# Kernel tuning notes

Measured on AMD Instinct MI355X. Metric: run time of the kernel, lower is better.

## Reference

```python
import jax, jax.numpy as jnp
import numpy as np

TEMPERATURE = 0.07


def setup_inputs() -> dict:
    key = jax.random.key(0)
    k1, k2, k3 = jax.random.split(key, 3)
    b, num_proposals, num_phrases, f = 128, 100, 16, 512
    img_features = jax.random.normal(k1, (b, num_proposals, f), dtype=jnp.float32)
    text_features = jax.random.normal(k2, (b, num_phrases, f), dtype=jnp.float32)
    labels = jax.random.randint(k3, (b, b), 0, 2, dtype=jnp.int64)
    return {"img_features": img_features, "text_features": text_features, "labels": labels}


def reference(img_features, text_features, labels):
    # att_matrix[b,d,t,i] = <text[b,t,:], img[d,i,:]>
    att_matrix = jnp.einsum('btf,dif->bdti', text_features, img_features)
    argmax_box = att_matrix.max(axis=3)        # [b, d, t]  max over proposals
    score_matrix = argmax_box.mean(axis=2)     # [b, d]     mean over phrases
    score_exp = jnp.exp(score_matrix / TEMPERATURE)
    return score_exp
```

## Files before the change

kernel.cpp:

```cpp
#include <hip/hip_runtime.h>
#include <hip/hip_bf16.h>
#include <stdint.h>


typedef __attribute__((ext_vector_type(4))) int   v4i;
typedef __attribute__((ext_vector_type(8))) int   v8i;
typedef __attribute__((ext_vector_type(4))) float f32x4;

constexpr int Bb = 128;
constexpr int P  = 100;
constexpr int T  = 16;
constexpr int F  = 512;
constexpr float TEMP = 0.07f;

constexpr int BM = 128;
constexpr int BK = 128;

__global__ void cvt_kernel(const float4* __restrict__ img, const float4* __restrict__ txt,
                           uint32_t* __restrict__ imgb, uint32_t* __restrict__ txtb,
                           int nimg4, int ntxt4) {
  const int stride = gridDim.x * blockDim.x;
  for (int i = blockIdx.x * blockDim.x + threadIdx.x; i < nimg4; i += stride) {
    float4 v = img[i];
    int w = __builtin_amdgcn_cvt_pk_fp8_f32(v.x, v.y, 0, false);
    w     = __builtin_amdgcn_cvt_pk_fp8_f32(v.z, v.w, w, true);
    imgb[i] = (uint32_t)w;
  }
  for (int i = blockIdx.x * blockDim.x + threadIdx.x; i < ntxt4; i += stride) {
    float4 v = txt[i];
    int w = __builtin_amdgcn_cvt_pk_fp8_f32(v.x, v.y, 0, false);
    w     = __builtin_amdgcn_cvt_pk_fp8_f32(v.z, v.w, w, true);
    txtb[i] = (uint32_t)w;
  }
}

template<bool FUSED>
__global__ __launch_bounds__(256)
void score_kernel(const void* __restrict__ imgp, const void* __restrict__ txtp,
                  float* __restrict__ out) {
  __shared__ __align__(16) unsigned char As[BM * BK];
  __shared__ __align__(16) unsigned char Bs[BM * BK];
  __shared__ float red[BM][2];

  const int d    = blockIdx.x;
  const int b0   = blockIdx.y * (BM / T);
  const int tid  = threadIdx.x;
  const int lane = tid & 63;
  const int w    = tid >> 6;
  const int q    = lane >> 4;
  const int n    = lane & 15;
  const int mh   = w & 1;
  const int nh   = w >> 1;

  f32x4 acc[4][4] = {};

  for (int kk = 0; kk < F; kk += BK) {
    if constexpr (!FUSED) {
      const uint8_t* gi = (const uint8_t*)imgp;
      const uint8_t* gt = (const uint8_t*)txtp;
      const int sub = lane >> 3;
      const int col = (((lane & 7) ^ sub) & 7) * 16;
      #pragma unroll
      for (int rr = 0; rr < 4; rr++) {
        const int c   = rr * 4 + w;
        const int row = c * 8 + sub;
        const uint8_t* ga = gt + (size_t)(b0 * T + row) * F + kk + col;
        __builtin_amdgcn_global_load_lds(
            (const __attribute__((address_space(1))) void*)ga,
            (__attribute__((address_space(3))) void*)&As[c * 1024], 16, 0, 0);
        const int prow = row < P ? row : 0;
        const uint8_t* gb = gi + ((size_t)d * P + prow) * F + kk + col;
        __builtin_amdgcn_global_load_lds(
            (const __attribute__((address_space(1))) void*)gb,
            (__attribute__((address_space(3))) void*)&Bs[c * 1024], 16, 0, 0);
      }
    } else {
      const float* gi = (const float*)imgp;
      const float* gt = (const float*)txtp;
      #pragma unroll
      for (int s = 0; s < 8; s++) {
        const int slot = s * 256 + tid;
        const int row  = slot >> 4;
        const int half = slot & 15;
        const int colf = half * 8;
        const int swz  = ((half >> 1) ^ (row & 7));
        const int offb = row * BK + swz * 16 + (half & 1) * 8;
        float4 v0 = *(const float4*)(gt + (size_t)(b0 * T + row) * F + kk + colf);
        float4 v1 = *(const float4*)(gt + (size_t)(b0 * T + row) * F + kk + colf + 4);
        int w0 = __builtin_amdgcn_cvt_pk_fp8_f32(v0.x, v0.y, 0, false);
        w0     = __builtin_amdgcn_cvt_pk_fp8_f32(v0.z, v0.w, w0, true);
        int w1 = __builtin_amdgcn_cvt_pk_fp8_f32(v1.x, v1.y, 0, false);
        w1     = __builtin_amdgcn_cvt_pk_fp8_f32(v1.z, v1.w, w1, true);
        *(uint2*)&As[offb] = make_uint2((uint32_t)w0, (uint32_t)w1);
        const int prow = row < P ? row : 0;
        float4 u0 = *(const float4*)(gi + ((size_t)d * P + prow) * F + kk + colf);
        float4 u1 = *(const float4*)(gi + ((size_t)d * P + prow) * F + kk + colf + 4);
        int x0 = __builtin_amdgcn_cvt_pk_fp8_f32(u0.x, u0.y, 0, false);
        x0     = __builtin_amdgcn_cvt_pk_fp8_f32(u0.z, u0.w, x0, true);
        int x1 = __builtin_amdgcn_cvt_pk_fp8_f32(u1.x, u1.y, 0, false);
        x1     = __builtin_amdgcn_cvt_pk_fp8_f32(u1.z, u1.w, x1, true);
        *(uint2*)&Bs[offb] = make_uint2((uint32_t)x0, (uint32_t)x1);
      }
    }
    __syncthreads();

    {
      const int k7 = n & 7;
      const int s0 = (2 * q) ^ k7;
      v8i a[4], bfr[4];
      #pragma unroll
      for (int rt = 0; rt < 4; rt++) {
        const int off = (mh * 64 + rt * 16 + n) * BK;
        v4i lo = *(const v4i*)&As[off + s0 * 16];
        v4i hi = *(const v4i*)&As[off + (s0 ^ 1) * 16];
        a[rt] = __builtin_shufflevector(lo, hi, 0, 1, 2, 3, 4, 5, 6, 7);
      }
      #pragma unroll
      for (int ct = 0; ct < 4; ct++) {
        const int off = (nh * 64 + ct * 16 + n) * BK;
        v4i lo = *(const v4i*)&Bs[off + s0 * 16];
        v4i hi = *(const v4i*)&Bs[off + (s0 ^ 1) * 16];
        bfr[ct] = __builtin_shufflevector(lo, hi, 0, 1, 2, 3, 4, 5, 6, 7);
      }
      #pragma unroll
      for (int rt = 0; rt < 4; rt++)
        #pragma unroll
        for (int ct = 0; ct < 4; ct++)
          acc[rt][ct] = __builtin_amdgcn_mfma_scale_f32_16x16x128_f8f6f4(
              a[rt], bfr[ct], acc[rt][ct], 0, 0, 0, 127, 0, 127);
    }
    __syncthreads();
  }

  #pragma unroll
  for (int rt = 0; rt < 4; rt++) {
    float m[4];
    #pragma unroll
    for (int r = 0; r < 4; r++) {
      float v = -3.0e38f;
      #pragma unroll
      for (int ct = 0; ct < 4; ct++) {
        const bool valid = (nh * 64 + ct * 16 + n) < P;
        const float x = acc[rt][ct][r];
        v = valid ? fmaxf(v, x) : v;
      }
      #pragma unroll
      for (int off = 1; off < 16; off <<= 1)
        v = fmaxf(v, __shfl_xor(v, off));
      m[r] = v;
    }
    if (n == 0) {
      #pragma unroll
      for (int r = 0; r < 4; r++)
        red[mh * 64 + rt * 16 + q * 4 + r][nh] = m[r];
    }
  }
  __syncthreads();

  if (tid < BM / T) {
    float s = 0.f;
    #pragma unroll
    for (int t = 0; t < T; t++) {
      const int r = tid * T + t;
      s += fmaxf(red[r][0], red[r][1]);
    }
    const float arg = fminf(s * (1.0f / (T * TEMP)), 88.0f);
    out[(size_t)(b0 + tid) * Bb + d] = expf(arg);
  }
}

extern "C" void kernel_launch(void* const* d_in, const int* in_sizes, int n_in,
                              void* d_out, int out_size, void* d_ws, size_t ws_size,
                              hipStream_t stream) {
  const float* img = (const float*)d_in[0];
  const float* txt = (const float*)d_in[1];
  float* out = (float*)d_out;

  const size_t imgN = (size_t)Bb * P * F;
  const size_t txtN = (size_t)Bb * T * F;
  const size_t need = imgN + txtN;

  dim3 grid(Bb, (Bb * T) / BM);
  if (ws_size >= need) {
    uint8_t* imgb = (uint8_t*)d_ws;
    uint8_t* txtb = imgb + imgN;
    cvt_kernel<<<2048, 256, 0, stream>>>((const float4*)img, (const float4*)txt,
                                         (uint32_t*)imgb, (uint32_t*)txtb,
                                         (int)(imgN / 4), (int)(txtN / 4));
    score_kernel<false><<<grid, 256, 0, stream>>>(imgb, txtb, out);
  } else {
    score_kernel<true><<<grid, 256, 0, stream>>>(img, txt, out);
  }
}
```

Measured before the change: 103.7 us.

## Double-buffer LDS tiles to overlap next K-slice loads with MFMA

```diff
diff --git a/kernel.cpp b/kernel.cpp
--- a/kernel.cpp
+++ b/kernel.cpp
@@ -15,6 +15,7 @@
 
 constexpr int BM = 128;
 constexpr int BK = 128;
+constexpr int NK = F / BK;
 
 __global__ void cvt_kernel(const float4* __restrict__ img, const float4* __restrict__ txt,
                            uint32_t* __restrict__ imgb, uint32_t* __restrict__ txtb,
@@ -38,8 +39,8 @@
 __global__ __launch_bounds__(256)
 void score_kernel(const void* __restrict__ imgp, const void* __restrict__ txtp,
                   float* __restrict__ out) {
-  __shared__ __align__(16) unsigned char As[BM * BK];
-  __shared__ __align__(16) unsigned char Bs[BM * BK];
+  __shared__ __align__(16) unsigned char As[2][BM * BK];
+  __shared__ __align__(16) unsigned char Bs[2][BM * BK];
   __shared__ float red[BM][2];
 
   const int d    = blockIdx.x;
@@ -54,7 +55,7 @@
 
   f32x4 acc[4][4] = {};
 
-  for (int kk = 0; kk < F; kk += BK) {
+  auto stage = [&](int buf, int kk) {
     if constexpr (!FUSED) {
       const uint8_t* gi = (const uint8_t*)imgp;
       const uint8_t* gt = (const uint8_t*)txtp;
@@ -67,12 +68,12 @@
         const uint8_t* ga = gt + (size_t)(b0 * T + row) * F + kk + col;
         __builtin_amdgcn_global_load_lds(
             (const __attribute__((address_space(1))) void*)ga,
-            (__attribute__((address_space(3))) void*)&As[c * 1024], 16, 0, 0);
+            (__attribute__((address_space(3))) void*)&As[buf][c * 1024], 16, 0, 0);
         const int prow = row < P ? row : 0;
         const uint8_t* gb = gi + ((size_t)d * P + prow) * F + kk + col;
         __builtin_amdgcn_global_load_lds(
             (const __attribute__((address_space(1))) void*)gb,
-            (__attribute__((address_space(3))) void*)&Bs[c * 1024], 16, 0, 0);
+            (__attribute__((address_space(3))) void*)&Bs[buf][c * 1024], 16, 0, 0);
       }
     } else {
       const float* gi = (const float*)imgp;
@@ -91,7 +92,7 @@
         w0     = __builtin_amdgcn_cvt_pk_fp8_f32(v0.z, v0.w, w0, true);
         int w1 = __builtin_amdgcn_cvt_pk_fp8_f32(v1.x, v1.y, 0, false);
         w1     = __builtin_amdgcn_cvt_pk_fp8_f32(v1.z, v1.w, w1, true);
-        *(uint2*)&As[offb] = make_uint2((uint32_t)w0, (uint32_t)w1);
+        *(uint2*)&As[buf][offb] = make_uint2((uint32_t)w0, (uint32_t)w1);
         const int prow = row < P ? row : 0;
         float4 u0 = *(const float4*)(gi + ((size_t)d * P + prow) * F + kk + colf);
         float4 u1 = *(const float4*)(gi + ((size_t)d * P + prow) * F + kk + colf + 4);
@@ -99,37 +100,43 @@
         x0     = __builtin_amdgcn_cvt_pk_fp8_f32(u0.z, u0.w, x0, true);
         int x1 = __builtin_amdgcn_cvt_pk_fp8_f32(u1.x, u1.y, 0, false);
         x1     = __builtin_amdgcn_cvt_pk_fp8_f32(u1.z, u1.w, x1, true);
-        *(uint2*)&Bs[offb] = make_uint2((uint32_t)x0, (uint32_t)x1);
+        *(uint2*)&Bs[buf][offb] = make_uint2((uint32_t)x0, (uint32_t)x1);
       }
     }
+  };
+
+  stage(0, 0);
+
+  #pragma unroll
+  for (int k4 = 0; k4 < NK; k4++) {
     __syncthreads();
-
-    {
-      const int k7 = n & 7;
-      const int s0 = (2 * q) ^ k7;
-      v8i a[4], bfr[4];
-      #pragma unroll
-      for (int rt = 0; rt < 4; rt++) {
-        const int off = (mh * 64 + rt * 16 + n) * BK;
-        v4i lo = *(const v4i*)&As[off + s0 * 16];
-        v4i hi = *(const v4i*)&As[off + (s0 ^ 1) * 16];
-        a[rt] = __builtin_shufflevector(lo, hi, 0, 1, 2, 3, 4, 5, 6, 7);
-      }
-      #pragma unroll
-      for (int ct = 0; ct < 4; ct++) {
-        const int off = (nh * 64 + ct * 16 + n) * BK;
-        v4i lo = *(const v4i*)&Bs[off + s0 * 16];
-        v4i hi = *(const v4i*)&Bs[off + (s0 ^ 1) * 16];
-        bfr[ct] = __builtin_shufflevector(lo, hi, 0, 1, 2, 3, 4, 5, 6, 7);
-      }
-      #pragma unroll
-      for (int rt = 0; rt < 4; rt++)
-        #pragma unroll
-        for (int ct = 0; ct < 4; ct++)
-          acc[rt][ct] = __builtin_amdgcn_mfma_scale_f32_16x16x128_f8f6f4(
-              a[rt], bfr[ct], acc[rt][ct], 0, 0, 0, 127, 0, 127);
-    }
-    __syncthreads();
+    if (k4 + 1 < NK) stage((k4 + 1) & 1, (k4 + 1) * BK);
+
+    const unsigned char* Ab = As[k4 & 1];
+    const unsigned char* Bbuf = Bs[k4 & 1];
+    const int k7 = n & 7;
+    const int s0 = (2 * q) ^ k7;
+    v8i a[4], bfr[4];
+    #pragma unroll
+    for (int rt = 0; rt < 4; rt++) {
+      const int off = (mh * 64 + rt * 16 + n) * BK;
+      v4i lo = *(const v4i*)&Ab[off + s0 * 16];
+      v4i hi = *(const v4i*)&Ab[off + (s0 ^ 1) * 16];
+      a[rt] = __builtin_shufflevector(lo, hi, 0, 1, 2, 3, 4, 5, 6, 7);
+    }
+    #pragma unroll
+    for (int ct = 0; ct < 4; ct++) {
+      const int off = (nh * 64 + ct * 16 + n) * BK;
+      v4i lo = *(const v4i*)&Bbuf[off + s0 * 16];
+      v4i hi = *(const v4i*)&Bbuf[off + (s0 ^ 1) * 16];
+      bfr[ct] = __builtin_shufflevector(lo, hi, 0, 1, 2, 3, 4, 5, 6, 7);
+    }
+    #pragma unroll
+    for (int rt = 0; rt < 4; rt++)
+      #pragma unroll
+      for (int ct = 0; ct < 4; ct++)
+        acc[rt][ct] = __builtin_amdgcn_mfma_scale_f32_16x16x128_f8f6f4(
+            a[rt], bfr[ct], acc[rt][ct], 0, 0, 0, 127, 0, 127);
   }
 
   #pragma unroll
```

Measured after the change: 100.5 us. 1.03x faster.

## Load fp8 MFMA operands directly from global memory, bypassing LDS staging

Applied to the files above, without the earlier changes.

```diff
diff --git a/kernel.cpp b/kernel.cpp
--- a/kernel.cpp
+++ b/kernel.cpp
@@ -12,9 +12,6 @@
 constexpr int T  = 16;
 constexpr int F  = 512;
 constexpr float TEMP = 0.07f;
-
-constexpr int BM = 128;
-constexpr int BK = 128;
 
 __global__ void cvt_kernel(const float4* __restrict__ img, const float4* __restrict__ txt,
                            uint32_t* __restrict__ imgb, uint32_t* __restrict__ txtb,
@@ -34,16 +31,12 @@
   }
 }
 
-template<bool FUSED>
 __global__ __launch_bounds__(256)
-void score_kernel(const void* __restrict__ imgp, const void* __restrict__ txtp,
+void score_direct(const uint8_t* __restrict__ gi, const uint8_t* __restrict__ gt,
                   float* __restrict__ out) {
-  __shared__ __align__(16) unsigned char As[BM * BK];
-  __shared__ __align__(16) unsigned char Bs[BM * BK];
-  __shared__ float red[BM][2];
+  __shared__ float red[128][2];
 
   const int d    = blockIdx.x;
-  const int b0   = blockIdx.y * (BM / T);
   const int tid  = threadIdx.x;
   const int lane = tid & 63;
   const int w    = tid >> 6;
@@ -52,84 +45,41 @@
   const int mh   = w & 1;
   const int nh   = w >> 1;
 
+  const uint8_t* aB[4];
+  const uint8_t* bB[4];
+  #pragma unroll
+  for (int rt = 0; rt < 4; rt++)
+    aB[rt] = gt + (size_t)(blockIdx.y * 128 + mh * 64 + rt * 16 + n) * F + q * 32;
+  #pragma unroll
+  for (int ct = 0; ct < 4; ct++) {
+    const int rl   = nh * 64 + ct * 16 + n;
+    const int prow = rl < P ? rl : 0;
+    bB[ct] = gi + ((size_t)d * P + prow) * F + q * 32;
+  }
+
   f32x4 acc[4][4] = {};
 
-  for (int kk = 0; kk < F; kk += BK) {
-    if constexpr (!FUSED) {
-      const uint8_t* gi = (const uint8_t*)imgp;
-      const uint8_t* gt = (const uint8_t*)txtp;
-      const int sub = lane >> 3;
-      const int col = (((lane & 7) ^ sub) & 7) * 16;
-      #pragma unroll
-      for (int rr = 0; rr < 4; rr++) {
-        const int c   = rr * 4 + w;
-        const int row = c * 8 + sub;
-        const uint8_t* ga = gt + (size_t)(b0 * T + row) * F + kk + col;
-        __builtin_amdgcn_global_load_lds(
-            (const __attribute__((address_space(1))) void*)ga,
-            (__attribute__((address_space(3))) void*)&As[c * 1024], 16, 0, 0);
-        const int prow = row < P ? row : 0;
-        const uint8_t* gb = gi + ((size_t)d * P + prow) * F + kk + col;
-        __builtin_amdgcn_global_load_lds(
-            (const __attribute__((address_space(1))) void*)gb,
-            (__attribute__((address_space(3))) void*)&Bs[c * 1024], 16, 0, 0);
-      }
-    } else {
-      const float* gi = (const float*)imgp;
-      const float* gt = (const float*)txtp;
-      #pragma unroll
-      for (int s = 0; s < 8; s++) {
-        const int slot = s * 256 + tid;
-        const int row  = slot >> 4;
-        const int half = slot & 15;
-        const int colf = half * 8;
-        const int swz  = ((half >> 1) ^ (row & 7));
-        const int offb = row * BK + swz * 16 + (half & 1) * 8;
-        float4 v0 = *(const float4*)(gt + (size_t)(b0 * T + row) * F + kk + colf);
-        float4 v1 = *(const float4*)(gt + (size_t)(b0 * T + row) * F + kk + colf + 4);
-        int w0 = __builtin_amdgcn_cvt_pk_fp8_f32(v0.x, v0.y, 0, false);
-        w0     = __builtin_amdgcn_cvt_pk_fp8_f32(v0.z, v0.w, w0, true);
-        int w1 = __builtin_amdgcn_cvt_pk_fp8_f32(v1.x, v1.y, 0, false);
-        w1     = __builtin_amdgcn_cvt_pk_fp8_f32(v1.z, v1.w, w1, true);
-        *(uint2*)&As[offb] = make_uint2((uint32_t)w0, (uint32_t)w1);
-        const int prow = row < P ? row : 0;
-        float4 u0 = *(const float4*)(gi + ((size_t)d * P + prow) * F + kk + colf);
-        float4 u1 = *(const float4*)(gi + ((size_t)d * P + prow) * F + kk + colf + 4);
-        int x0 = __builtin_amdgcn_cvt_pk_fp8_f32(u0.x, u0.y, 0, false);
-        x0     = __builtin_amdgcn_cvt_pk_fp8_f32(u0.z, u0.w, x0, true);
-        int x1 = __builtin_amdgcn_cvt_pk_fp8_f32(u1.x, u1.y, 0, false);
-        x1     = __builtin_amdgcn_cvt_pk_fp8_f32(u1.z, u1.w, x1, true);
-        *(uint2*)&Bs[offb] = make_uint2((uint32_t)x0, (uint32_t)x1);
-      }
-    }
-    __syncthreads();
-
-    {
-      const int k7 = n & 7;
-      const int s0 = (2 * q) ^ k7;
-      v8i a[4], bfr[4];
-      #pragma unroll
-      for (int rt = 0; rt < 4; rt++) {
-        const int off = (mh * 64 + rt * 16 + n) * BK;
-        v4i lo = *(const v4i*)&As[off + s0 * 16];
-        v4i hi = *(const v4i*)&As[off + (s0 ^ 1) * 16];
-        a[rt] = __builtin_shufflevector(lo, hi, 0, 1, 2, 3, 4, 5, 6, 7);
-      }
-      #pragma unroll
-      for (int ct = 0; ct < 4; ct++) {
-        const int off = (nh * 64 + ct * 16 + n) * BK;
-        v4i lo = *(const v4i*)&Bs[off + s0 * 16];
-        v4i hi = *(const v4i*)&Bs[off + (s0 ^ 1) * 16];
-        bfr[ct] = __builtin_shufflevector(lo, hi, 0, 1, 2, 3, 4, 5, 6, 7);
-      }
-      #pragma unroll
-      for (int rt = 0; rt < 4; rt++)
-        #pragma unroll
-        for (int ct = 0; ct < 4; ct++)
-          acc[rt][ct] = __builtin_amdgcn_mfma_scale_f32_16x16x128_f8f6f4(
-              a[rt], bfr[ct], acc[rt][ct], 0, 0, 0, 127, 0, 127);
-    }
-    __syncthreads();
+  #pragma unroll
+  for (int kk = 0; kk < F; kk += 128) {
+    v8i a[4], b[4];
+    #pragma unroll
+    for (int rt = 0; rt < 4; rt++) {
+      v4i lo = *(const v4i*)(aB[rt] + kk);
+      v4i hi = *(const v4i*)(aB[rt] + kk + 16);
+      a[rt] = __builtin_shufflevector(lo, hi, 0, 1, 2, 3, 4, 5, 6, 7);
+    }
+    #pragma unroll
+    for (int ct = 0; ct < 4; ct++) {
+      v4i lo = *(const v4i*)(bB[ct] + kk);
+      v4i hi = *(const v4i*)(bB[ct] + kk + 16);
+      b[ct] = __builtin_shufflevector(lo, hi, 0, 1, 2, 3, 4, 5, 6, 7);
+    }
+    #pragma unroll
+    for (int rt = 0; rt < 4; rt++)
+      #pragma unroll
+      for (int ct = 0; ct < 4; ct++)
+        acc[rt][ct] = __builtin_amdgcn_mfma_scale_f32_16x16x128_f8f6f4(
+            a[rt], b[ct], acc[rt][ct], 0, 0, 0, 127, 0, 127);
   }
 
   #pragma unroll
@@ -157,7 +107,116 @@
   }
   __syncthreads();
 
-  if (tid < BM / T) {
+  if (tid < 8) {
+    float s = 0.f;
+    #pragma unroll
+    for (int t = 0; t < T; t++) {
+      const int r = tid * T + t;
+      s += fmaxf(red[r][0], red[r][1]);
+    }
+    const float arg = fminf(s * (1.0f / (T * TEMP)), 88.0f);
+    out[(size_t)(blockIdx.y * 8 + tid) * Bb + d] = expf(arg);
+  }
+}
+
+__global__ __launch_bounds__(256)
+void score_fallback(const float* __restrict__ gi, const float* __restrict__ gt,
+                    float* __restrict__ out) {
+  __shared__ __align__(16) unsigned char As[128 * 128];
+  __shared__ __align__(16) unsigned char Bs[128 * 128];
+  __shared__ float red[128][2];
+
+  const int d    = blockIdx.x;
+  const int b0   = blockIdx.y * 8;
+  const int tid  = threadIdx.x;
+  const int lane = tid & 63;
+  const int q    = lane >> 4;
+  const int n    = lane & 15;
+  const int w    = tid >> 6;
+  const int mh   = w & 1;
+  const int nh   = w >> 1;
+
+  f32x4 acc[4][4] = {};
+
+  for (int kk = 0; kk < F; kk += 128) {
+    #pragma unroll
+    for (int s = 0; s < 8; s++) {
+      const int slot = s * 256 + tid;
+      const int row  = slot >> 4;
+      const int half = slot & 15;
+      const int colf = half * 8;
+      const int swz  = ((half >> 1) ^ (row & 7));
+      const int offb = row * 128 + swz * 16 + (half & 1) * 8;
+      float4 v0 = *(const float4*)(gt + (size_t)(b0 * T + row) * F + kk + colf);
+      float4 v1 = *(const float4*)(gt + (size_t)(b0 * T + row) * F + kk + colf + 4);
+      int w0 = __builtin_amdgcn_cvt_pk_fp8_f32(v0.x, v0.y, 0, false);
+      w0     = __builtin_amdgcn_cvt_pk_fp8_f32(v0.z, v0.w, w0, true);
+      int w1 = __builtin_amdgcn_cvt_pk_fp8_f32(v1.x, v1.y, 0, false);
+      w1     = __builtin_amdgcn_cvt_pk_fp8_f32(v1.z, v1.w, w1, true);
+      *(uint2*)&As[offb] = make_uint2((uint32_t)w0, (uint32_t)w1);
+      const int prow = row < P ? row : 0;
+      float4 u0 = *(const float4*)(gi + ((size_t)d * P + prow) * F + kk + colf);
+      float4 u1 = *(const float4*)(gi + ((size_t)d * P + prow) * F + kk + colf + 4);
+      int x0 = __builtin_amdgcn_cvt_pk_fp8_f32(u0.x, u0.y, 0, false);
+      x0     = __builtin_amdgcn_cvt_pk_fp8_f32(u0.z, u0.w, x0, true);
+      int x1 = __builtin_amdgcn_cvt_pk_fp8_f32(u1.x, u1.y, 0, false);
+      x1     = __builtin_amdgcn_cvt_pk_fp8_f32(u1.z, u1.w, x1, true);
+      *(uint2*)&Bs[offb] = make_uint2((uint32_t)x0, (uint32_t)x1);
+    }
+    __syncthreads();
+
+    const int k7 = n & 7;
+    const int s0 = (2 * q) ^ k7;
+    v8i a[4], bfr[4];
+    #pragma unroll
+    for (int rt = 0; rt < 4; rt++) {
+      const int off = (mh * 64 + rt * 16 + n) * 128;
+      v4i lo = *(const v4i*)&As[off + s0 * 16];
+      v4i hi = *(const v4i*)&As[off + (s0 ^ 1) * 16];
+      a[rt] = __builtin_shufflevector(lo, hi, 0, 1, 2, 3, 4, 5, 6, 7);
+    }
+    #pragma unroll
+    for (int ct = 0; ct < 4; ct++) {
+      const int off = (nh * 64 + ct * 16 + n) * 128;
+      v4i lo = *(const v4i*)&Bs[off + s0 * 16];
+      v4i hi = *(const v4i*)&Bs[off + (s0 ^ 1) * 16];
+      bfr[ct] = __builtin_shufflevector(lo, hi, 0, 1, 2, 3, 4, 5, 6, 7);
+    }
+    #pragma unroll
+    for (int rt = 0; rt < 4; rt++)
+      #pragma unroll
+      for (int ct = 0; ct < 4; ct++)
+        acc[rt][ct] = __builtin_amdgcn_mfma_scale_f32_16x16x128_f8f6f4(
+            a[rt], bfr[ct], acc[rt][ct], 0, 0, 0, 127, 0, 127);
+    __syncthreads();
+  }
+
+  #pragma unroll
+  for (int rt = 0; rt < 4; rt++) {
+    float m[4];
+    #pragma unroll
+    for (int r = 0; r < 4; r++) {
+      float v = -3.0e38f;
+      #pragma unroll
+      for (int ct = 0; ct < 4; ct++) {
+        const bool valid = (nh * 64 + ct * 16 + n) < P;
+        const float x = acc[rt][ct][r];
+        v = valid ? fmaxf(v, x) : v;
+      }
+      #pragma unroll
+      for (int off = 1; off < 16; off <<= 1)
+        v = fmaxf(v, __shfl_xor(v, off));
+      m[r] = v;
+    }
+    if (n == 0) {
+      #pragma unroll
+      for (int r = 0; r < 4; r++)
+        red[mh * 64 + rt * 16 + q * 4 + r][nh] = m[r];
+    }
+  }
+  __syncthreads();
+
+  if (tid < 8) {
     float s = 0.f;
     #pragma unroll
     for (int t = 0; t < T; t++) {
@@ -180,15 +239,15 @@
   const size_t txtN = (size_t)Bb * T * F;
   const size_t need = imgN + txtN;
 
-  dim3 grid(Bb, (Bb * T) / BM);
+  dim3 grid(Bb, (Bb * T) / 128);
   if (ws_size >= need) {
     uint8_t* imgb = (uint8_t*)d_ws;
     uint8_t* txtb = imgb + imgN;
     cvt_kernel<<<2048, 256, 0, stream>>>((const float4*)img, (const float4*)txt,
                                          (uint32_t*)imgb, (uint32_t*)txtb,
                                          (int)(imgN / 4), (int)(txtN / 4));
-    score_kernel<false><<<grid, 256, 0, stream>>>(imgb, txtb, out);
+    score_direct<<<grid, 256, 0, stream>>>(imgb, txtb, out);
   } else {
-    score_kernel<true><<<grid, 256, 0, stream>>>(img, txt, out);
-  }
-}
+    score_fallback<<<grid, 256, 0, stream>>>(img, txt, out);
+  }
+}
```

Measured after the change: 129.9 us. 25.2% more time.
